# Optimization experiments

Hardware: AMD Instinct MI355X
Metric: run time of the kernel (lower is better)

The kernel has to match this reference:

```python
import jax, jax.numpy as jnp
import numpy as np

LOG2E = 1.44269504

def setup_inputs() -> dict:
    key = jax.random.key(0)
    kq, kk, kv = jax.random.split(key, 3)
    shape = (4, 16, 2048, 128)  # [batch, heads, seq, head_dim]
    return {
        "query": jax.random.normal(kq, shape, dtype=jnp.float32),
        "key": jax.random.normal(kk, shape, dtype=jnp.float32),
        "value": jax.random.normal(kv, shape, dtype=jnp.float32),
    }

def reference(query, key, value):
    head_dim = query.shape[-1]
    scale_factor = 1.0 / (head_dim ** 0.5)  # scale=None path in the torch module
    scaled_q = query * (scale_factor * LOG2E)
    # [b,h,s,d] x [b,h,t,d] -> [b,h,s,t]
    attn_scores = jnp.einsum('bhsd,bhtd->bhst', scaled_q, key)
    attn_weights = jax.nn.softmax(attn_scores, axis=-1)
    # [b,h,s,t] x [b,h,t,d] -> [b,h,s,d]
    return jnp.einsum('bhst,bhtd->bhsd', attn_weights, value)
```

## Files before the change

### kernel.cpp

```cpp
#include <hip/hip_runtime.h>
#include <hip/hip_bf16.h>
#include <stdint.h>

typedef short v8s __attribute__((ext_vector_type(8)));
typedef short v4s __attribute__((ext_vector_type(4)));
typedef float v4f __attribute__((ext_vector_type(4)));

constexpr int S     = 2048;
constexpr int D     = 128;
constexpr int QBLK  = 64;
constexpr int KVBLK = 64;
constexpr int NT    = S / KVBLK;
constexpr int BH    = 64;

#define LOG2E_F 1.44269504f

__device__ __forceinline__ unsigned short f2bf(float x) {
    union { float f; uint32_t u; } v; v.f = x;
    uint32_t r = v.u + 0x7FFFu + ((v.u >> 16) & 1u);
    return (unsigned short)(r >> 16);
}

__device__ __forceinline__ void gload_lds16(const void* g, void* l) {
    __builtin_amdgcn_global_load_lds(
        (const __attribute__((address_space(1))) unsigned int*)g,
        (__attribute__((address_space(3))) unsigned int*)l,
        16, 0, 0);
}

__global__ __launch_bounds__(256)
void kconv_kernel(const float* __restrict__ src, short* __restrict__ dst) {
    size_t i = ((size_t)blockIdx.x * 256 + threadIdx.x) * 8;
    float4 a = *(const float4*)(src + i);
    float4 b = *(const float4*)(src + i + 4);
    v8s t;
    t[0] = (short)f2bf(a.x); t[1] = (short)f2bf(a.y);
    t[2] = (short)f2bf(a.z); t[3] = (short)f2bf(a.w);
    t[4] = (short)f2bf(b.x); t[5] = (short)f2bf(b.y);
    t[6] = (short)f2bf(b.z); t[7] = (short)f2bf(b.w);
    *(v8s*)(dst + i) = t;
}

__global__ __launch_bounds__(256)
void vtrans_kernel(const float* __restrict__ Vg, short* __restrict__ VtG) {
    __shared__ __align__(16) short T[D * KVBLK];
    const int bh = blockIdx.y;
    const int kv0 = blockIdx.x * KVBLK;
    const float* vp = Vg + ((size_t)bh * S + kv0) * D;
    const int kv = threadIdx.x >> 2;
    const int dg = threadIdx.x & 3;
    #pragma unroll
    for (int s4 = 0; s4 < 4; ++s4) {
        float4 a = *(const float4*)(vp + (size_t)kv * D + s4 * 32 + dg * 8);
        float4 b = *(const float4*)(vp + (size_t)kv * D + s4 * 32 + dg * 8 + 4);
        float vv[8] = {a.x, a.y, a.z, a.w, b.x, b.y, b.z, b.w};
        #pragma unroll
        for (int j = 0; j < 8; ++j) {
            int d = s4 * 32 + dg * 8 + j;
            T[d * KVBLK + (kv ^ ((d & 7) << 3))] = (short)f2bf(vv[j]);
        }
    }
    __syncthreads();
    const int s = threadIdx.x & 7;
    #pragma unroll
    for (int p = 0; p < 4; ++p) {
        int d = p * 32 + (threadIdx.x >> 3);
        v8s w = *(const v8s*)(&T[d * KVBLK + ((s ^ (d & 7)) << 3)]);
        *(v8s*)(VtG + (size_t)bh * D * S + (size_t)d * S + kv0 + s * 8) = w;
    }
}

__global__ __launch_bounds__(256, 2)
void fattn_kernel(const float* __restrict__ Qg,
                  const short* __restrict__ Kb,
                  const short* __restrict__ Vb,
                  float* __restrict__ Og)
{
    __shared__ __align__(16) short Ks[2][KVBLK * D];
    __shared__ __align__(16) short Vt[2][D * KVBLK];
    __shared__ __align__(16) short Pl[4][16 * KVBLK];

    const int tid  = threadIdx.x;
    const int wave = tid >> 6;
    const int lane = tid & 63;
    const int l15  = lane & 15;
    const int lg   = lane >> 4;

    const int bid = blockIdx.x;
    const int swz = ((bid & 7) << 8) | (bid >> 3);
    const int bh  = swz >> 5;
    const int qt  = swz & 31;
    const int q0  = qt * QBLK + wave * 16;
    const size_t base = (size_t)bh * S * D;

    const float SCALE = LOG2E_F * LOG2E_F * 0.08838834764831845f;

    v8s qf[4];
    {
        const float* qp = Qg + base + (size_t)(q0 + l15) * D + lg * 8;
        #pragma unroll
        for (int dc = 0; dc < 4; ++dc) {
            float4 a = *(const float4*)(qp + dc * 32);
            float4 b = *(const float4*)(qp + dc * 32 + 4);
            v8s t;
            t[0] = (short)f2bf(a.x * SCALE); t[1] = (short)f2bf(a.y * SCALE);
            t[2] = (short)f2bf(a.z * SCALE); t[3] = (short)f2bf(a.w * SCALE);
            t[4] = (short)f2bf(b.x * SCALE); t[5] = (short)f2bf(b.y * SCALE);
            t[6] = (short)f2bf(b.z * SCALE); t[7] = (short)f2bf(b.w * SCALE);
            qf[dc] = t;
        }
    }

    const v4f zf = {0.f, 0.f, 0.f, 0.f};
    v4f o[8];
    #pragma unroll
    for (int i = 0; i < 8; ++i) o[i] = zf;
    float m_run = -1e30f;
    float l_run = 0.f;

    auto stage = [&](int buf, int kv0) {
        #pragma unroll
        for (int i = 0; i < 4; ++i) {
            int rb  = wave * 4 + i;
            int row = rb * 4 + (lane >> 4);
            int s   = lane & 15;
            const short* src = Kb + base + (size_t)(kv0 + row) * D + ((s ^ (row & 7)) << 3);
            gload_lds16(src, &Ks[buf][rb * 512]);
        }
        #pragma unroll
        for (int i = 0; i < 4; ++i) {
            int rb = wave * 4 + i;
            int d  = rb * 8 + (lane >> 3);
            int s  = lane & 7;
            int sz = (d & 7) ^ (((d >> 3) & 3) << 1);
            const short* src = Vb + base + (size_t)d * S + kv0 + ((s ^ sz) << 3);
            gload_lds16(src, &Vt[buf][rb * 512]);
        }
    };

    stage(0, 0);
    __syncthreads();

    for (int it = 0; it < NT; ++it) {
        const int c = it & 1;
        if (it + 1 < NT) stage(c ^ 1, (it + 1) * KVBLK);

        const short* ks = &Ks[c][0];
        const short* vt = &Vt[c][0];

        v4f sc[4];
        #pragma unroll
        for (int t = 0; t < 4; ++t) sc[t] = zf;
        __builtin_amdgcn_s_setprio(1);
        #pragma unroll
        for (int t = 0; t < 4; ++t) {
            int row = t * 16 + l15;
            #pragma unroll
            for (int dc = 0; dc < 4; ++dc) {
                int cg = dc * 4 + lg;
                v8s kf = *(const v8s*)(&ks[row * D + ((cg ^ (row & 7)) << 3)]);
                sc[t] = __builtin_amdgcn_mfma_f32_16x16x32_bf16(kf, qf[dc], sc[t], 0, 0, 0);
            }
        }
        __builtin_amdgcn_s_setprio(0);

        float tm = sc[0][0];
        #pragma unroll
        for (int t = 0; t < 4; ++t)
            #pragma unroll
            for (int r = 0; r < 4; ++r) tm = fmaxf(tm, sc[t][r]);
        tm = fmaxf(tm, __shfl_xor(tm, 16));
        tm = fmaxf(tm, __shfl_xor(tm, 32));
        float m_new = fmaxf(m_run, tm);
        float alpha = exp2f(m_run - m_new);

        float tsum = 0.f;
        v4s pv[4];
        #pragma unroll
        for (int t = 0; t < 4; ++t) {
            #pragma unroll
            for (int r = 0; r < 4; ++r) {
                float p = exp2f(sc[t][r] - m_new);
                tsum += p;
                pv[t][r] = (short)f2bf(p);
            }
        }
        tsum += __shfl_xor(tsum, 16);
        tsum += __shfl_xor(tsum, 32);
        l_run = l_run * alpha + tsum;
        m_run = m_new;
        #pragma unroll
        for (int i = 0; i < 8; ++i) o[i] = o[i] * alpha;

        short* pw = &Pl[wave][0];
        #pragma unroll
        for (int t = 0; t < 4; ++t) {
            int kvb = t * 16 + lg * 4;
            int idx = l15 * KVBLK + (((kvb >> 3) ^ (l15 & 7)) << 3) + (kvb & 7);
            *(v4s*)(&pw[idx]) = pv[t];
        }
        v8s pf[2];
        #pragma unroll
        for (int h = 0; h < 2; ++h) {
            int kvg = h * 4 + lg;
            pf[h] = *(const v8s*)(&pw[l15 * KVBLK + ((kvg ^ (l15 & 7)) << 3)]);
        }

        __builtin_amdgcn_s_setprio(1);
        #pragma unroll
        for (int ds = 0; ds < 8; ++ds) {
            int d  = ds * 16 + l15;
            int sw = ((d & 7) << 3) ^ (((d >> 3) & 3) << 4);
            #pragma unroll
            for (int h = 0; h < 2; ++h) {
                v8s vf = *(const v8s*)(&vt[d * KVBLK + ((h * 32 + lg * 8) ^ sw)]);
                o[ds] = __builtin_amdgcn_mfma_f32_16x16x32_bf16(vf, pf[h], o[ds], 0, 0, 0);
            }
        }
        __builtin_amdgcn_s_setprio(0);

        __syncthreads();
    }

    float inv = 1.f / l_run;
    float* op = Og + base + (size_t)(q0 + l15) * D;
    #pragma unroll
    for (int ds = 0; ds < 8; ++ds) {
        float4 w;
        w.x = o[ds][0] * inv; w.y = o[ds][1] * inv;
        w.z = o[ds][2] * inv; w.w = o[ds][3] * inv;
        *(float4*)(op + ds * 16 + lg * 4) = w;
    }
}

extern "C" void kernel_launch(void* const* d_in, const int* in_sizes, int n_in,
                              void* d_out, int out_size, void* d_ws, size_t ws_size,
                              hipStream_t stream) {
    const float* Q = (const float*)d_in[0];
    const float* K = (const float*)d_in[1];
    const float* V = (const float*)d_in[2];
    float* O = (float*)d_out;

    short* Kb  = (short*)d_ws;
    short* VtG = Kb + (size_t)BH * S * D;

    kconv_kernel<<<dim3(BH * S * D / (256 * 8)), dim3(256), 0, stream>>>(K, Kb);
    vtrans_kernel<<<dim3(S / KVBLK, BH), dim3(256), 0, stream>>>(V, VtG);

    fattn_kernel<<<dim3(BH * S / QBLK), dim3(256), 0, stream>>>(Q, Kb, VtG, O);
}
```

Measured before the change: 460.7 us.

## Rewrite attention with 32x32 MFMA, in-register P, lazy rescale, fused prep

Switches QK and PV to 32x32x16 bf16 MFMA with 8 waves of 32 queries each, so each block covers 256 queries and the K/V tiles are reused by more rows. The P operand is built in registers with packed bf16 conversion and permlane32 swaps, which removes the LDS round-trip for P. Output rescaling is skipped when the running max grows by at most 8 (the log2-domain threshold), and the K conversion and V transpose are merged into one prep kernel. In exchange there are fewer blocks (512) and higher register pressure, and the lazy rescale allows unnormalized exponentials up to 2^8, which may affect accuracy.

```diff
diff --git a/kernel.cpp b/kernel.cpp
--- a/kernel.cpp
+++ b/kernel.cpp
@@ -3,15 +3,11 @@
 #include <stdint.h>
 
 typedef short v8s __attribute__((ext_vector_type(8)));
-typedef short v4s __attribute__((ext_vector_type(4)));
-typedef float v4f __attribute__((ext_vector_type(4)));
-
-constexpr int S     = 2048;
-constexpr int D     = 128;
-constexpr int QBLK  = 64;
-constexpr int KVBLK = 64;
-constexpr int NT    = S / KVBLK;
-constexpr int BH    = 64;
+typedef float v16f __attribute__((ext_vector_type(16)));
+typedef unsigned int u32;
+
+constexpr int S = 2048, D = 128, KVBLK = 64, NT = S / KVBLK, BH = 64;
+constexpr int QW = 32, WAVES = 8, QBLK = QW * WAVES;
 
 #define LOG2E_F 1.44269504f
 
@@ -20,121 +16,117 @@
     uint32_t r = v.u + 0x7FFFu + ((v.u >> 16) & 1u);
     return (unsigned short)(r >> 16);
 }
-
+__device__ __forceinline__ u32 cvtpk(float lo, float hi) {
+    u32 r; asm("v_cvt_pk_bf16_f32 %0, %1, %2" : "=v"(r) : "v"(lo), "v"(hi)); return r;
+}
 __device__ __forceinline__ void gload_lds16(const void* g, void* l) {
     __builtin_amdgcn_global_load_lds(
         (const __attribute__((address_space(1))) unsigned int*)g,
-        (__attribute__((address_space(3))) unsigned int*)l,
-        16, 0, 0);
+        (__attribute__((address_space(3))) unsigned int*)l, 16, 0, 0);
 }
 
 __global__ __launch_bounds__(256)
-void kconv_kernel(const float* __restrict__ src, short* __restrict__ dst) {
-    size_t i = ((size_t)blockIdx.x * 256 + threadIdx.x) * 8;
-    float4 a = *(const float4*)(src + i);
-    float4 b = *(const float4*)(src + i + 4);
-    v8s t;
-    t[0] = (short)f2bf(a.x); t[1] = (short)f2bf(a.y);
-    t[2] = (short)f2bf(a.z); t[3] = (short)f2bf(a.w);
-    t[4] = (short)f2bf(b.x); t[5] = (short)f2bf(b.y);
-    t[6] = (short)f2bf(b.z); t[7] = (short)f2bf(b.w);
-    *(v8s*)(dst + i) = t;
-}
-
-__global__ __launch_bounds__(256)
-void vtrans_kernel(const float* __restrict__ Vg, short* __restrict__ VtG) {
+void prep_kernel(const float* __restrict__ Kg, const float* __restrict__ Vg,
+                 short* __restrict__ Kb, short* __restrict__ VtG)
+{
     __shared__ __align__(16) short T[D * KVBLK];
-    const int bh = blockIdx.y;
-    const int kv0 = blockIdx.x * KVBLK;
-    const float* vp = Vg + ((size_t)bh * S + kv0) * D;
-    const int kv = threadIdx.x >> 2;
-    const int dg = threadIdx.x & 3;
-    #pragma unroll
-    for (int s4 = 0; s4 < 4; ++s4) {
-        float4 a = *(const float4*)(vp + (size_t)kv * D + s4 * 32 + dg * 8);
-        float4 b = *(const float4*)(vp + (size_t)kv * D + s4 * 32 + dg * 8 + 4);
-        float vv[8] = {a.x, a.y, a.z, a.w, b.x, b.y, b.z, b.w};
-        #pragma unroll
-        for (int j = 0; j < 8; ++j) {
-            int d = s4 * 32 + dg * 8 + j;
-            T[d * KVBLK + (kv ^ ((d & 7) << 3))] = (short)f2bf(vv[j]);
-        }
-    }
-    __syncthreads();
-    const int s = threadIdx.x & 7;
-    #pragma unroll
-    for (int p = 0; p < 4; ++p) {
-        int d = p * 32 + (threadIdx.x >> 3);
-        v8s w = *(const v8s*)(&T[d * KVBLK + ((s ^ (d & 7)) << 3)]);
-        *(v8s*)(VtG + (size_t)bh * D * S + (size_t)d * S + kv0 + s * 8) = w;
-    }
-}
-
-__global__ __launch_bounds__(256, 2)
-void fattn_kernel(const float* __restrict__ Qg,
-                  const short* __restrict__ Kb,
-                  const short* __restrict__ Vb,
-                  float* __restrict__ Og)
+    const int bh = blockIdx.y, kv0 = blockIdx.x * KVBLK;
+    const int tid = threadIdx.x;
+    {
+        const float* kp = Kg + ((size_t)bh * S + kv0) * D;
+        short* kb = Kb + ((size_t)bh * S + kv0) * D;
+        #pragma unroll
+        for (int i = 0; i < 4; ++i) {
+            int e = (i * 256 + tid) * 8;
+            float4 a = *(const float4*)(kp + e), b = *(const float4*)(kp + e + 4);
+            v8s t;
+            t[0] = f2bf(a.x); t[1] = f2bf(a.y); t[2] = f2bf(a.z); t[3] = f2bf(a.w);
+            t[4] = f2bf(b.x); t[5] = f2bf(b.y); t[6] = f2bf(b.z); t[7] = f2bf(b.w);
+            *(v8s*)(kb + e) = t;
+        }
+    }
+    {
+        const float* vp = Vg + ((size_t)bh * S + kv0) * D;
+        const int kv = tid >> 2, dg = tid & 3;
+        #pragma unroll
+        for (int s4 = 0; s4 < 4; ++s4) {
+            float4 a = *(const float4*)(vp + (size_t)kv * D + s4 * 32 + dg * 8);
+            float4 b = *(const float4*)(vp + (size_t)kv * D + s4 * 32 + dg * 8 + 4);
+            float vv[8] = {a.x, a.y, a.z, a.w, b.x, b.y, b.z, b.w};
+            #pragma unroll
+            for (int j = 0; j < 8; ++j) {
+                int d = s4 * 32 + dg * 8 + j;
+                T[d * KVBLK + (kv ^ ((d & 7) << 3))] = (short)f2bf(vv[j]);
+            }
+        }
+        __syncthreads();
+        const int s = tid & 7;
+        #pragma unroll
+        for (int p = 0; p < 4; ++p) {
+            int d = p * 32 + (tid >> 3);
+            v8s w = *(const v8s*)(&T[d * KVBLK + ((s ^ (d & 7)) << 3)]);
+            *(v8s*)(VtG + (size_t)bh * D * S + (size_t)d * S + kv0 + s * 8) = w;
+        }
+    }
+}
+
+__global__ __launch_bounds__(512, 2)
+void fattn_kernel(const float* __restrict__ Qg, const short* __restrict__ Kb,
+                  const short* __restrict__ Vb, float* __restrict__ Og)
 {
     __shared__ __align__(16) short Ks[2][KVBLK * D];
     __shared__ __align__(16) short Vt[2][D * KVBLK];
-    __shared__ __align__(16) short Pl[4][16 * KVBLK];
-
-    const int tid  = threadIdx.x;
-    const int wave = tid >> 6;
-    const int lane = tid & 63;
-    const int l15  = lane & 15;
-    const int lg   = lane >> 4;
+
+    const int tid = threadIdx.x, wave = tid >> 6, lane = tid & 63;
+    const int l31 = lane & 31, h = lane >> 5;
 
     const int bid = blockIdx.x;
-    const int swz = ((bid & 7) << 8) | (bid >> 3);
-    const int bh  = swz >> 5;
-    const int qt  = swz & 31;
-    const int q0  = qt * QBLK + wave * 16;
+    const int bh = (bid & 7) | ((bid >> 6) << 3);
+    const int qt = (bid >> 3) & 7;
+    const int q0 = qt * QBLK + wave * QW;
     const size_t base = (size_t)bh * S * D;
 
     const float SCALE = LOG2E_F * LOG2E_F * 0.08838834764831845f;
 
-    v8s qf[4];
+    v8s qf[8];
     {
-        const float* qp = Qg + base + (size_t)(q0 + l15) * D + lg * 8;
-        #pragma unroll
-        for (int dc = 0; dc < 4; ++dc) {
-            float4 a = *(const float4*)(qp + dc * 32);
-            float4 b = *(const float4*)(qp + dc * 32 + 4);
-            v8s t;
-            t[0] = (short)f2bf(a.x * SCALE); t[1] = (short)f2bf(a.y * SCALE);
-            t[2] = (short)f2bf(a.z * SCALE); t[3] = (short)f2bf(a.w * SCALE);
-            t[4] = (short)f2bf(b.x * SCALE); t[5] = (short)f2bf(b.y * SCALE);
-            t[6] = (short)f2bf(b.z * SCALE); t[7] = (short)f2bf(b.w * SCALE);
-            qf[dc] = t;
-        }
-    }
-
-    const v4f zf = {0.f, 0.f, 0.f, 0.f};
-    v4f o[8];
+        const float* qp = Qg + base + (size_t)(q0 + l31) * D + h * 8;
+        #pragma unroll
+        for (int kst = 0; kst < 8; ++kst) {
+            float4 a = *(const float4*)(qp + kst * 16);
+            float4 b = *(const float4*)(qp + kst * 16 + 4);
+            union { u32 w[4]; v8s v; } qu;
+            qu.w[0] = cvtpk(a.x * SCALE, a.y * SCALE);
+            qu.w[1] = cvtpk(a.z * SCALE, a.w * SCALE);
+            qu.w[2] = cvtpk(b.x * SCALE, b.y * SCALE);
+            qu.w[3] = cvtpk(b.z * SCALE, b.w * SCALE);
+            qf[kst] = qu.v;
+        }
+    }
+
+    v16f o[4];
     #pragma unroll
-    for (int i = 0; i < 8; ++i) o[i] = zf;
-    float m_run = -1e30f;
-    float l_run = 0.f;
+    for (int i = 0; i < 4; ++i)
+        #pragma unroll
+        for (int r = 0; r < 16; ++r) o[i][r] = 0.f;
+    float m_run = -1e30f, l_run = 0.f;
 
     auto stage = [&](int buf, int kv0) {
         #pragma unroll
-        for (int i = 0; i < 4; ++i) {
-            int rb  = wave * 4 + i;
-            int row = rb * 4 + (lane >> 4);
-            int s   = lane & 15;
-            const short* src = Kb + base + (size_t)(kv0 + row) * D + ((s ^ (row & 7)) << 3);
-            gload_lds16(src, &Ks[buf][rb * 512]);
-        }
-        #pragma unroll
-        for (int i = 0; i < 4; ++i) {
-            int rb = wave * 4 + i;
-            int d  = rb * 8 + (lane >> 3);
-            int s  = lane & 7;
-            int sz = (d & 7) ^ (((d >> 3) & 3) << 1);
-            const short* src = Vb + base + (size_t)d * S + kv0 + ((s ^ sz) << 3);
-            gload_lds16(src, &Vt[buf][rb * 512]);
+        for (int i = 0; i < 2; ++i) {
+            int ch = wave * 2 + i;
+            int row = ch * 4 + (lane >> 4);
+            int sl = lane & 15;
+            const short* src = Kb + base + (size_t)(kv0 + row) * D + ((sl ^ (row & 7)) << 3);
+            gload_lds16(src, &Ks[buf][ch * 512]);
+        }
+        #pragma unroll
+        for (int i = 0; i < 2; ++i) {
+            int ch = wave * 2 + i;
+            int d = ch * 8 + (lane >> 3);
+            int sl = lane & 7;
+            const short* src = Vb + base + (size_t)d * S + kv0 + ((sl ^ (d & 7)) << 3);
+            gload_lds16(src, &Vt[buf][ch * 512]);
         }
     };
 
@@ -148,89 +140,89 @@
         const short* ks = &Ks[c][0];
         const short* vt = &Vt[c][0];
 
-        v4f sc[4];
-        #pragma unroll
-        for (int t = 0; t < 4; ++t) sc[t] = zf;
+        v16f s0, s1;
+        #pragma unroll
+        for (int r = 0; r < 16; ++r) { s0[r] = 0.f; s1[r] = 0.f; }
         __builtin_amdgcn_s_setprio(1);
         #pragma unroll
-        for (int t = 0; t < 4; ++t) {
-            int row = t * 16 + l15;
+        for (int kst = 0; kst < 8; ++kst) {
+            int sl = (kst * 2 + h) ^ (l31 & 7);
+            v8s k0 = *(const v8s*)(&ks[l31 * D + sl * 8]);
+            s0 = __builtin_amdgcn_mfma_f32_32x32x16_bf16(k0, qf[kst], s0, 0, 0, 0);
+            v8s k1 = *(const v8s*)(&ks[(32 + l31) * D + sl * 8]);
+            s1 = __builtin_amdgcn_mfma_f32_32x32x16_bf16(k1, qf[kst], s1, 0, 0, 0);
+        }
+        __builtin_amdgcn_s_setprio(0);
+
+        float tm = s0[0];
+        #pragma unroll
+        for (int r = 1; r < 16; ++r) tm = fmaxf(tm, s0[r]);
+        #pragma unroll
+        for (int r = 0; r < 16; ++r) tm = fmaxf(tm, s1[r]);
+        tm = fmaxf(tm, __shfl_xor(tm, 32));
+
+        bool skip = __all(tm <= m_run + 8.f);
+        if (!skip) {
+            float m_new = fmaxf(m_run, tm);
+            float alpha = exp2f(m_run - m_new);
             #pragma unroll
-            for (int dc = 0; dc < 4; ++dc) {
-                int cg = dc * 4 + lg;
-                v8s kf = *(const v8s*)(&ks[row * D + ((cg ^ (row & 7)) << 3)]);
-                sc[t] = __builtin_amdgcn_mfma_f32_16x16x32_bf16(kf, qf[dc], sc[t], 0, 0, 0);
+            for (int i = 0; i < 4; ++i)
+                #pragma unroll
+                for (int r = 0; r < 16; ++r) o[i][r] *= alpha;
+            l_run *= alpha;
+            m_run = m_new;
+        }
+        float ts = 0.f;
+        #pragma unroll
+        for (int r = 0; r < 16; ++r) { s0[r] = exp2f(s0[r] - m_run); ts += s0[r]; }
+        #pragma unroll
+        for (int r = 0; r < 16; ++r) { s1[r] = exp2f(s1[r] - m_run); ts += s1[r]; }
+        ts += __shfl_xor(ts, 32);
+        l_run += ts;
+
+        v8s pf[4];
+        #pragma unroll
+        for (int ks2 = 0; ks2 < 4; ++ks2) {
+            const v16f& P = (ks2 < 2) ? s0 : s1;
+            int rb = (ks2 & 1) * 8;
+            u32 a  = cvtpk(P[rb + 0], P[rb + 1]);
+            u32 b  = cvtpk(P[rb + 2], P[rb + 3]);
+            u32 cc = cvtpk(P[rb + 4], P[rb + 5]);
+            u32 dd = cvtpk(P[rb + 6], P[rb + 7]);
+            asm volatile("v_permlane32_swap_b32 %0, %1" : "+v"(a), "+v"(cc));
+            asm volatile("v_permlane32_swap_b32 %0, %1" : "+v"(b), "+v"(dd));
+            union { u32 w[4]; v8s v; } pu;
+            pu.w[0] = a; pu.w[1] = b; pu.w[2] = cc; pu.w[3] = dd;
+            pf[ks2] = pu.v;
+        }
+
+        __builtin_amdgcn_s_setprio(1);
+        #pragma unroll
+        for (int dt = 0; dt < 4; ++dt) {
+            int d = dt * 32 + l31;
+            #pragma unroll
+            for (int ks2 = 0; ks2 < 4; ++ks2) {
+                int sl = (ks2 * 2 + h) ^ (d & 7);
+                v8s vf = *(const v8s*)(&vt[d * KVBLK + sl * 8]);
+                o[dt] = __builtin_amdgcn_mfma_f32_32x32x16_bf16(vf, pf[ks2], o[dt], 0, 0, 0);
             }
         }
         __builtin_amdgcn_s_setprio(0);
 
-        float tm = sc[0][0];
-        #pragma unroll
-        for (int t = 0; t < 4; ++t)
-            #pragma unroll
-            for (int r = 0; r < 4; ++r) tm = fmaxf(tm, sc[t][r]);
-        tm = fmaxf(tm, __shfl_xor(tm, 16));
-        tm = fmaxf(tm, __shfl_xor(tm, 32));
-        float m_new = fmaxf(m_run, tm);
-        float alpha = exp2f(m_run - m_new);
-
-        float tsum = 0.f;
-        v4s pv[4];
-        #pragma unroll
-        for (int t = 0; t < 4; ++t) {
-            #pragma unroll
-            for (int r = 0; r < 4; ++r) {
-                float p = exp2f(sc[t][r] - m_new);
-                tsum += p;
-                pv[t][r] = (short)f2bf(p);
-            }
-        }
-        tsum += __shfl_xor(tsum, 16);
-        tsum += __shfl_xor(tsum, 32);
-        l_run = l_run * alpha + tsum;
-        m_run = m_new;
-        #pragma unroll
-        for (int i = 0; i < 8; ++i) o[i] = o[i] * alpha;
-
-        short* pw = &Pl[wave][0];
-        #pragma unroll
-        for (int t = 0; t < 4; ++t) {
-            int kvb = t * 16 + lg * 4;
-            int idx = l15 * KVBLK + (((kvb >> 3) ^ (l15 & 7)) << 3) + (kvb & 7);
-            *(v4s*)(&pw[idx]) = pv[t];
-        }
-        v8s pf[2];
-        #pragma unroll
-        for (int h = 0; h < 2; ++h) {
-            int kvg = h * 4 + lg;
-            pf[h] = *(const v8s*)(&pw[l15 * KVBLK + ((kvg ^ (l15 & 7)) << 3)]);
-        }
-
-        __builtin_amdgcn_s_setprio(1);
-        #pragma unroll
-        for (int ds = 0; ds < 8; ++ds) {
-            int d  = ds * 16 + l15;
-            int sw = ((d & 7) << 3) ^ (((d >> 3) & 3) << 4);
-            #pragma unroll
-            for (int h = 0; h < 2; ++h) {
-                v8s vf = *(const v8s*)(&vt[d * KVBLK + ((h * 32 + lg * 8) ^ sw)]);
-                o[ds] = __builtin_amdgcn_mfma_f32_16x16x32_bf16(vf, pf[h], o[ds], 0, 0, 0);
-            }
-        }
-        __builtin_amdgcn_s_setprio(0);
-
         __syncthreads();
     }
 
     float inv = 1.f / l_run;
-    float* op = Og + base + (size_t)(q0 + l15) * D;
+    float* op = Og + base + (size_t)(q0 + l31) * D;
     #pragma unroll
-    for (int ds = 0; ds < 8; ++ds) {
-        float4 w;
-        w.x = o[ds][0] * inv; w.y = o[ds][1] * inv;
-        w.z = o[ds][2] * inv; w.w = o[ds][3] * inv;
-        *(float4*)(op + ds * 16 + lg * 4) = w;
-    }
+    for (int dt = 0; dt < 4; ++dt)
+        #pragma unroll
+        for (int g = 0; g < 4; ++g) {
+            float4 w;
+            w.x = o[dt][g * 4 + 0] * inv; w.y = o[dt][g * 4 + 1] * inv;
+            w.z = o[dt][g * 4 + 2] * inv; w.w = o[dt][g * 4 + 3] * inv;
+            *(float4*)(op + dt * 32 + g * 8 + 4 * h) = w;
+        }
 }
 
 extern "C" void kernel_launch(void* const* d_in, const int* in_sizes, int n_in,
@@ -244,8 +236,6 @@
     short* Kb  = (short*)d_ws;
     short* VtG = Kb + (size_t)BH * S * D;
 
-    kconv_kernel<<<dim3(BH * S * D / (256 * 8)), dim3(256), 0, stream>>>(K, Kb);
-    vtrans_kernel<<<dim3(S / KVBLK, BH), dim3(256), 0, stream>>>(V, VtG);
-
-    fattn_kernel<<<dim3(BH * S / QBLK), dim3(256), 0, stream>>>(Q, Kb, VtG, O);
-}
+    prep_kernel<<<dim3(NT, BH), dim3(256), 0, stream>>>(K, V, Kb, VtG);
+    fattn_kernel<<<dim3(BH * 8), dim3(512), 0, stream>>>(Q, Kb, VtG, O);
+}
```

New measurement: 393.6 us. -14.6%, faster.
